# Performance work log

Hardware: AMD Instinct MI355X
Metric: run time of the kernel (lower is better)

## Reference

```python
import jax, jax.numpy as jnp
import numpy as np

N = 100000  # nodes
E = 1600000  # edges (before self-loops)
F_IN, F_HID, F_OUT = 64, 128, 64


def setup_inputs() -> dict:
    key = jax.random.key(0)
    ks = jax.random.split(key, 8)
    x = jax.random.normal(ks[0], (N, F_IN), dtype=jnp.float32)
    edge_index = jax.random.randint(ks[1], (2, E), 0, N, dtype=jnp.int64)
    # Glorot-ish init for weights, zero bias (PyG GCNConv default)
    W1 = jax.random.normal(ks[2], (F_IN, F_HID), dtype=jnp.float32) / np.sqrt(F_IN)
    W2 = jax.random.normal(ks[3], (F_HID, F_HID), dtype=jnp.float32) / np.sqrt(F_HID)
    W3 = jax.random.normal(ks[4], (F_HID, F_OUT), dtype=jnp.float32) / np.sqrt(F_HID)
    b1 = jnp.zeros((F_HID,), dtype=jnp.float32)
    b2 = jnp.zeros((F_HID,), dtype=jnp.float32)
    b3 = jnp.zeros((F_OUT,), dtype=jnp.float32)
    return {"x": x, "edge_index": edge_index, "W1": W1, "b1": b1,
            "W2": W2, "b2": b2, "W3": W3, "b3": b3}


def _gcn_norm(edge_index, num_nodes):
    """Add self-loops and compute symmetric D^-1/2 A D^-1/2 edge norms."""
    loop = jnp.arange(num_nodes, dtype=edge_index.dtype)
    src = jnp.concatenate([edge_index[0], loop])  # [E+N]
    dst = jnp.concatenate([edge_index[1], loop])  # [E+N]
    deg = jax.ops.segment_sum(jnp.ones_like(src, dtype=jnp.float32), dst,
                              num_segments=num_nodes)
    dinv = jnp.where(deg > 0, jax.lax.rsqrt(deg), 0.0)
    norm = dinv[src] * dinv[dst]  # [E+N]
    return src, dst, norm


def _gcn_conv(h, src, dst, norm, W, b, num_nodes):
    hw = h @ W                                   # [N, out] dense transform
    msg = hw[src] * norm[:, None]                # gather + edge scale
    out = jax.ops.segment_sum(msg, dst, num_segments=num_nodes)  # scatter-add
    return out + b


def reference(x, edge_index, W1, b1, W2, b2, W3, b3):
    src, dst, norm = _gcn_norm(edge_index, N)
    h = jax.nn.relu(_gcn_conv(x, src, dst, norm, W1, b1, N))
    h = jax.nn.relu(_gcn_conv(h, src, dst, norm, W2, b2, N))
    return _gcn_conv(h, src, dst, norm, W3, b3, N)
```

## Files before the change

kernel.cpp:

```cpp
#include <hip/hip_runtime.h>
#include <hip/hip_bf16.h>
#include <hip/hip_fp16.h>


typedef _Float16 h8 __attribute__((ext_vector_type(8)));
typedef float f4 __attribute__((ext_vector_type(4)));

constexpr int BSHIFT = 7;
constexpr int BNODES = 1 << BSHIFT;
constexpr int PB     = 256;
constexpr int CAP    = 4096;

__device__ inline void load8h(const _Float16* p, float* f) {
    h8 v = *(const h8*)p;
#pragma unroll
    for (int j = 0; j < 8; j++) f[j] = (float)v[j];
}

__device__ inline void store8h(_Float16* p, const float* f) {
    h8 v;
#pragma unroll
    for (int j = 0; j < 8; j++) v[j] = (_Float16)f[j];
    *(h8*)p = v;
}

__device__ inline void store4h(_Float16* p, float4 v) {
    _Float16 t[4] = {(_Float16)v.x, (_Float16)v.y, (_Float16)v.z, (_Float16)v.w};
    *(uint2*)p = *(uint2*)t;
}

__global__ __launch_bounds__(256) void phist_k(const int* __restrict__ dst,
                                               int* __restrict__ hist,
                                               int E, int nbuck, int chunk) {
    __shared__ int h[1024];
    for (int i = threadIdx.x; i < nbuck; i += 256) h[i] = 0;
    __syncthreads();
    int beg = blockIdx.x * chunk;
    int end = min(E, beg + chunk);
    for (int e = beg + threadIdx.x; e < end; e += 256)
        atomicAdd(&h[dst[e] >> BSHIFT], 1);
    __syncthreads();
    for (int i = threadIdx.x; i < nbuck; i += 256)
        hist[(long)blockIdx.x * nbuck + i] = h[i];
}

__global__ __launch_bounds__(256) void scan_blocks_k(const int* __restrict__ in,
                                                     int* __restrict__ excl,
                                                     int* __restrict__ bsums, int n) {
    __shared__ int s[256];
    int tid = threadIdx.x;
    int i = blockIdx.x * 256 + tid;
    int v = (i < n) ? in[i] : 0;
    s[tid] = v;
    __syncthreads();
    for (int off = 1; off < 256; off <<= 1) {
        int t = (tid >= off) ? s[tid - off] : 0;
        __syncthreads();
        s[tid] += t;
        __syncthreads();
    }
    if (i < n) excl[i] = s[tid] - v;
    if (tid == 255) bsums[blockIdx.x] = s[255];
}

__global__ __launch_bounds__(1024) void mid_k(int* __restrict__ bsums, int nb,
                                              const int* __restrict__ hist,
                                              int* __restrict__ bbase,
                                              int nbuck, int E) {
    __shared__ int s[1024];
    int tid = threadIdx.x;
    int v = 0;
    if (blockIdx.x == 0) {
        v = (tid < nb) ? bsums[tid] : 0;
    } else {
        if (tid < nbuck) {
            int t0 = 0, t1 = 0, t2 = 0, t3 = 0;
            for (int j = 0; j < PB; j += 4) {
                t0 += hist[(long)(j + 0) * nbuck + tid];
                t1 += hist[(long)(j + 1) * nbuck + tid];
                t2 += hist[(long)(j + 2) * nbuck + tid];
                t3 += hist[(long)(j + 3) * nbuck + tid];
            }
            v = (t0 + t1) + (t2 + t3);
        }
    }
    s[tid] = v;
    __syncthreads();
    for (int off = 1; off < 1024; off <<= 1) {
        int t = (tid >= off) ? s[tid - off] : 0;
        __syncthreads();
        s[tid] += t;
        __syncthreads();
    }
    if (blockIdx.x == 0) {
        if (tid < nb) bsums[tid] = s[tid] - v;
    } else {
        if (tid < nbuck) bbase[tid] = s[tid] - v;
        if (tid == 0) bbase[nbuck] = E;
    }
}

__global__ __launch_bounds__(256) void part2_k(const int* __restrict__ src,
                                               const int* __restrict__ dst,
                                               const int* __restrict__ offs,
                                               const int* __restrict__ bsums,
                                               unsigned* __restrict__ ebuf,
                                               int E, int nbuck, int chunk) {
    __shared__ int cur[1024];
    for (int i = threadIdx.x; i < nbuck; i += 256) {
        long flat = (long)blockIdx.x * nbuck + i;
        cur[i] = offs[flat] + bsums[flat >> 8];
    }
    __syncthreads();
    int beg = blockIdx.x * chunk;
    int end = min(E, beg + chunk);
    for (int e = beg + threadIdx.x; e < end; e += 256) {
        int d = dst[e];
        int b = d >> BSHIFT;
        int pos = atomicAdd(&cur[b], 1);
        ebuf[pos] = ((unsigned)(d & (BNODES - 1)) << 25) | (unsigned)src[e];
    }
}

__global__ __launch_bounds__(256) void finalize_k(const unsigned* __restrict__ ebuf,
                                                  const int* __restrict__ hist,
                                                  const int* __restrict__ offs,
                                                  const int* __restrict__ bsums,
                                                  const int* __restrict__ bbase,
                                                  int nbuck,
                                                  int* __restrict__ rowst,
                                                  int* __restrict__ rowend,
                                                  int* __restrict__ midp,
                                                  float* __restrict__ dinv,
                                                  int* __restrict__ col,
                                                  const float* __restrict__ x,
                                                  _Float16* __restrict__ msgX,
                                                  int N, int H) {
    __shared__ unsigned se[CAP];
    __shared__ int cj[PB], sj[PB], sb[PB];
    __shared__ int cnt_s[BNODES], cntA_s[BNODES], scan_s[BNODES];
    __shared__ int cur_s[BNODES], curB_s[BNODES];
    __shared__ float di_s[BNODES];

    int b = blockIdx.x, tid = threadIdx.x;
    int node0 = b << BSHIFT;
    int nn = min(BNODES, N - node0);
    int beg = bbase[b];

    if (tid < PB) {
        long flat = (long)tid * nbuck + b;
        cj[tid] = hist[flat];
        sj[tid] = offs[flat] + bsums[flat >> 8];
    }
    if (tid < BNODES) { cnt_s[tid] = 0; cntA_s[tid] = 0; }
    __syncthreads();

    if (tid < PB) sb[tid] = cj[tid];
    __syncthreads();
    for (int off = 1; off < PB; off <<= 1) {
        int t = 0;
        if (tid < PB && tid >= off) t = sb[tid - off];
        __syncthreads();
        if (tid < PB) sb[tid] += t;
        __syncthreads();
    }
    int m = sb[PB - 1];
    __syncthreads();

    {
        int j = tid;
        int base = sb[j] - cj[j], c = cj[j], s0 = sj[j];
        for (int k = 0; k < c; k++) {
            unsigned e = ebuf[s0 + k];
            int idx = base + k;
            if (idx < CAP) se[idx] = e;
            else {
                atomicAdd(&cnt_s[e >> 25], 1);
                if ((int)(e & 0x1FFFFFFu) < H) atomicAdd(&cntA_s[e >> 25], 1);
            }
        }
    }
    __syncthreads();

    int mcap = m < CAP ? m : CAP;
    for (int i = tid; i < mcap; i += 256) {
        unsigned e = se[i];
        atomicAdd(&cnt_s[e >> 25], 1);
        if ((int)(e & 0x1FFFFFFu) < H) atomicAdd(&cntA_s[e >> 25], 1);
    }
    __syncthreads();

    int v = (tid < BNODES) ? cnt_s[tid] : 0;
    if (tid < BNODES) scan_s[tid] = v;
    __syncthreads();
    for (int off = 1; off < BNODES; off <<= 1) {
        int t = 0;
        if (tid < BNODES && tid >= off) t = scan_s[tid - off];
        __syncthreads();
        if (tid < BNODES) scan_s[tid] += t;
        __syncthreads();
    }
    if (tid < nn) {
        int ex = scan_s[tid] - v;
        int st = beg + ex;
        int ca = cntA_s[tid];
        rowst[node0 + tid] = st;
        rowend[node0 + tid] = st + v;
        midp[node0 + tid] = st + ca;
        float di = rsqrtf((float)v + 1.0f);
        dinv[node0 + tid] = di;
        di_s[tid] = di;
        cur_s[tid] = ex;
        curB_s[tid] = ex + ca;
    }
    __syncthreads();

    for (int i = tid; i < mcap; i += 256) {
        unsigned e = se[i];
        int s = (int)(e & 0x1FFFFFFu), d = e >> 25;
        int p = (s < H) ? atomicAdd(&cur_s[d], 1) : atomicAdd(&curB_s[d], 1);
        col[beg + p] = s;
    }
    if (m > CAP) {
        int j = tid;
        int base = sb[j] - cj[j], c = cj[j], s0 = sj[j];
        for (int k = 0; k < c; k++) {
            int idx = base + k;
            if (idx >= CAP) {
                unsigned e = ebuf[s0 + k];
                int s = (int)(e & 0x1FFFFFFu), d = e >> 25;
                int p = (s < H) ? atomicAdd(&cur_s[d], 1) : atomicAdd(&curB_s[d], 1);
                col[beg + p] = s;
            }
        }
    }

    for (int t = tid; t < nn * 16; t += 256) {
        int nl = t >> 4, q = t & 15;
        int node = node0 + nl;
        float4 vx = *(const float4*)(x + (long)node * 64 + q * 4);
        float di = di_s[nl];
        vx.x *= di; vx.y *= di; vx.z *= di; vx.w *= di;
        store4h(msgX + (long)node * 64 + q * 4, vx);
    }
}

template <int K, int FOUT, bool BIAS, bool RELU, bool DINV_OUT, bool SMOUT>
__global__ __launch_bounds__(256) void fag_k(const _Float16* __restrict__ msg,
                                             const int* __restrict__ rowst,
                                             const int* __restrict__ rowend,
                                             const int* __restrict__ col,
                                             const float* __restrict__ dinv,
                                             const _Float16* __restrict__ Wsw,
                                             const float* __restrict__ bias,
                                             _Float16* __restrict__ C, int n) {
    constexpr int NT = FOUT / 16, NC = K / 32;
    constexpr int LDK = K + 8;
    constexpr int LPN = K / 8;
    constexpr int NPB = 256 / LPN;
    constexpr int CC = 2560;
    __shared__ _Float16 As[64 * LDK];
    __shared__ int cls[CC];

    int tid = threadIdx.x;
    int row0 = blockIdx.x * 64;

    int lastn = min(row0 + 64, n) - 1;
    int beg0 = rowst[row0];
    int win  = rowend[lastn] - beg0;
    int wl = min(win, CC);
    for (int i = tid; i < wl; i += 256) cls[i] = col[beg0 + i];
    __syncthreads();
    const int* cb = (win <= CC) ? (const int*)cls : (col + beg0);

#pragma unroll
    for (int pass = 0; pass < 64 / NPB; pass++) {
        int nl = pass * NPB + tid / LPN;
        int q = tid % LPN;
        int node = row0 + nl;
        float acc[8];
        if (node < n) {
            load8h(msg + (long)node * K + q * 8, acc);
            int beg = rowst[node] - beg0, end = rowend[node] - beg0;
            int e = beg;
            for (; e + 4 <= end; e += 4) {
                int s0 = cb[e], s1 = cb[e + 1], s2 = cb[e + 2], s3 = cb[e + 3];
                h8 v0 = *(const h8*)(msg + (long)s0 * K + q * 8);
                h8 v1 = *(const h8*)(msg + (long)s1 * K + q * 8);
                h8 v2 = *(const h8*)(msg + (long)s2 * K + q * 8);
                h8 v3 = *(const h8*)(msg + (long)s3 * K + q * 8);
#pragma unroll
                for (int j = 0; j < 8; j++)
                    acc[j] += ((float)v0[j] + (float)v1[j]) + ((float)v2[j] + (float)v3[j]);
            }
            for (; e < end; e++) {
                int s = cb[e];
                h8 v = *(const h8*)(msg + (long)s * K + q * 8);
#pragma unroll
                for (int j = 0; j < 8; j++) acc[j] += (float)v[j];
            }
            float di = dinv[node];
#pragma unroll
            for (int j = 0; j < 8; j++) acc[j] *= di;
        } else {
#pragma unroll
            for (int j = 0; j < 8; j++) acc[j] = 0.f;
        }
        h8 o;
#pragma unroll
        for (int j = 0; j < 8; j++) o[j] = (_Float16)acc[j];
        *(h8*)(As + nl * LDK + q * 8) = o;
    }
    __syncthreads();

    int lane = tid & 63, wave = tid >> 6;
    int quad = lane >> 4, cl = lane & 15;
    int r0 = wave * 16;

    h8 a[NC];
#pragma unroll
    for (int c = 0; c < NC; c++)
        a[c] = *(const h8*)(As + (r0 + cl) * LDK + quad * 8 + c * 32);

    f4 acc2[NT];
#pragma unroll
    for (int t = 0; t < NT; t++) acc2[t] = (f4){0.f, 0.f, 0.f, 0.f};

    const h8* wv = (const h8*)Wsw;
#pragma unroll
    for (int c = 0; c < NC; c++) {
#pragma unroll
        for (int t = 0; t < NT; t++)
            acc2[t] = __builtin_amdgcn_mfma_f32_16x16x32_f16(
                a[c], wv[(c * NT + t) * 64 + lane], acc2[t], 0, 0, 0);
    }

#pragma unroll
    for (int t = 0; t < NT; t++) {
        int c0 = t * 16 + cl;
        float bb = BIAS ? bias[c0] : 0.f;
#pragma unroll
        for (int r = 0; r < 4; r++) {
            int row = row0 + r0 + quad * 4 + r;
            if (row >= n) continue;
            float v = acc2[t][r] + bb;
            if (RELU) v = fmaxf(v, 0.f);
            if (DINV_OUT) v *= dinv[row];
            if (SMOUT)
                C[((long)(t >> 1) * n + row) * 32 + (t & 1) * 16 + cl] = (_Float16)v;
            else
                C[(long)row * FOUT + c0] = (_Float16)v;
        }
    }
}

__global__ __launch_bounds__(256) void agg_h2_k(const _Float16* __restrict__ msg,
                                                const int* __restrict__ rowst,
                                                const int* __restrict__ midp,
                                                const int* __restrict__ rowend,
                                                const int* __restrict__ col,
                                                _Float16* __restrict__ part, int n) {
    constexpr int CC = 1536;
    __shared__ int cls[CC];
    int idx7  = blockIdx.x & 7;
    int slice = idx7 & 3, half = idx7 >> 2;
    int blk   = blockIdx.x >> 3;
    int tid   = threadIdx.x;
    int node0b = blk * 32;

    int lastn = min(node0b + 32, n) - 1;
    int beg0 = rowst[node0b];
    int win  = rowend[lastn] - beg0;
    int wl = min(win, CC);
    for (int i = tid; i < wl; i += 256) cls[i] = col[beg0 + i];
    __syncthreads();
    const int* cb = (win <= CC) ? (const int*)cls : (col + beg0);

    int node  = node0b + (tid >> 3);
    int eslot = (tid >> 2) & 1;
    int q     = tid & 3;
    if (node >= n) return;
    const _Float16* mp = msg + (long)slice * n * 32 + q * 8;

    float acc[8];
#pragma unroll
    for (int j = 0; j < 8; j++) acc[j] = 0.f;

    int beg = (half ? midp[node] : rowst[node]) - beg0;
    int end = (half ? rowend[node] : midp[node]) - beg0;
    int e = beg + eslot;
    for (; e + 6 < end; e += 8) {
        int s0 = cb[e], s1 = cb[e + 2], s2 = cb[e + 4], s3 = cb[e + 6];
        h8 v0 = *(const h8*)(mp + (long)s0 * 32);
        h8 v1 = *(const h8*)(mp + (long)s1 * 32);
        h8 v2 = *(const h8*)(mp + (long)s2 * 32);
        h8 v3 = *(const h8*)(mp + (long)s3 * 32);
#pragma unroll
        for (int j = 0; j < 8; j++)
            acc[j] += (((float)v0[j] + (float)v1[j]) + ((float)v2[j] + (float)v3[j]));
    }
    for (; e < end; e += 2) {
        int s = cb[e];
        h8 v = *(const h8*)(mp + (long)s * 32);
#pragma unroll
        for (int j = 0; j < 8; j++) acc[j] += (float)v[j];
    }

#pragma unroll
    for (int j = 0; j < 8; j++) acc[j] += __shfl_xor(acc[j], 4);

    if (eslot == 0) {
        store8h(part + (((long)half * 4 + slice) * n + node) * 32 + q * 8, acc);
    }
}

template <int F, bool BIAS, bool F16OUT>
__global__ __launch_bounds__(256) void agg_f16_k(const _Float16* __restrict__ msg,
                                                 const int* __restrict__ rowst,
                                                 const int* __restrict__ rowend,
                                                 const int* __restrict__ col,
                                                 const float* __restrict__ dinv,
                                                 const float* __restrict__ b,
                                                 void* __restrict__ out, int n) {
    constexpr int LPN = F / 8;
    constexpr int NPB = 256 / LPN;
    constexpr int CC = NPB * 48;
    __shared__ int cls[CC];
    int tid = threadIdx.x;
    int node0b = blockIdx.x * NPB;

    int lastn = min(node0b + NPB, n) - 1;
    int beg0 = rowst[node0b];
    int win  = rowend[lastn] - beg0;
    int wl = min(win, CC);
    for (int i = tid; i < wl; i += 256) cls[i] = col[beg0 + i];
    __syncthreads();
    const int* cb = (win <= CC) ? (const int*)cls : (col + beg0);

    int node = node0b + tid / LPN;
    int q = tid % LPN;
    if (node >= n) return;

    float acc[8];
    load8h(msg + (long)node * F + q * 8, acc);

    int beg = rowst[node] - beg0, end = rowend[node] - beg0;
    int e = beg;
    for (; e + 8 <= end; e += 8) {
        h8 v[8];
#pragma unroll
        for (int u = 0; u < 8; u++)
            v[u] = *(const h8*)(msg + (long)cb[e + u] * F + q * 8);
#pragma unroll
        for (int j = 0; j < 8; j++)
            acc[j] += (((float)v[0][j] + (float)v[1][j]) + ((float)v[2][j] + (float)v[3][j])) +
                      (((float)v[4][j] + (float)v[5][j]) + ((float)v[6][j] + (float)v[7][j]));
    }
    for (; e + 4 <= end; e += 4) {
        h8 v0 = *(const h8*)(msg + (long)cb[e] * F + q * 8);
        h8 v1 = *(const h8*)(msg + (long)cb[e + 1] * F + q * 8);
        h8 v2 = *(const h8*)(msg + (long)cb[e + 2] * F + q * 8);
        h8 v3 = *(const h8*)(msg + (long)cb[e + 3] * F + q * 8);
#pragma unroll
        for (int j = 0; j < 8; j++)
            acc[j] += ((float)v0[j] + (float)v1[j]) + ((float)v2[j] + (float)v3[j]);
    }
    for (; e < end; e++) {
        h8 v = *(const h8*)(msg + (long)cb[e] * F + q * 8);
#pragma unroll
        for (int j = 0; j < 8; j++) acc[j] += (float)v[j];
    }

    float di = dinv[node];
    float o[8];
#pragma unroll
    for (int j = 0; j < 8; j++) o[j] = di * acc[j];
    if (BIAS) {
#pragma unroll
        for (int j = 0; j < 8; j++) o[j] += b[q * 8 + j];
    }
    if (F16OUT) {
        store8h((_Float16*)out + (long)node * F + q * 8, o);
    } else {
        float* dst = (float*)out + (long)node * F + q * 8;
        *(float4*)dst = make_float4(o[0], o[1], o[2], o[3]);
        *(float4*)(dst + 4) = make_float4(o[4], o[5], o[6], o[7]);
    }
}

template <int K, int FOUT>
__device__ inline void wfrag(const float* __restrict__ W,
                             _Float16* __restrict__ Wsw, int t) {
    constexpr int NT = FOUT / 16;
    int lane = t & 63;
    int tile = (t >> 6) % NT;
    int chunk = (t >> 6) / NT;
    int kbase = chunk * 32 + (lane >> 4) * 8;
    int nc = tile * 16 + (lane & 15);
    h8 v;
#pragma unroll
    for (int j = 0; j < 8; j++) v[j] = (_Float16)W[(kbase + j) * FOUT + nc];
    ((h8*)Wsw)[t] = v;
}

__global__ __launch_bounds__(256) void wprep3_k(const float* __restrict__ W1,
                                                const float* __restrict__ W2,
                                                const float* __restrict__ W3,
                                                _Float16* __restrict__ w1s,
                                                _Float16* __restrict__ w2s,
                                                _Float16* __restrict__ w3s) {
    int t = blockIdx.x * 256 + threadIdx.x;
    if (t < 1024) wfrag<64, 128>(W1, w1s, t);
    else if (t < 3072) wfrag<128, 128>(W2, w2s, t - 1024);
    else if (t < 4096) wfrag<128, 64>(W3, w3s, t - 3072);
}

__global__ __launch_bounds__(256) void dgemm_k(const _Float16* __restrict__ part,
                                               const _Float16* __restrict__ selfm,
                                               const _Float16* __restrict__ w2s,
                                               const _Float16* __restrict__ w3s,
                                               const float* __restrict__ b2,
                                               const float* __restrict__ dinv,
                                               _Float16* __restrict__ C, int n) {
    constexpr int LDK = 136;
    __shared__ _Float16 Hs[64 * LDK];

    int tid = threadIdx.x, lane = tid & 63, wave = tid >> 6;
    int quad = lane >> 4, cl = lane & 15;
    int row0 = blockIdx.x * 64, r0 = wave * 16;
    int arow = row0 + r0 + cl;

    const _Float16* pA = part;
    const _Float16* pB = part + (long)4 * n * 32;
    float di = dinv[arow];

    h8 a[4];
#pragma unroll
    for (int c = 0; c < 4; c++) {
        long off = ((long)c * n + arow) * 32 + quad * 8;
        h8 va = *(const h8*)(pA + off);
        h8 vb = *(const h8*)(pB + off);
        h8 vs = *(const h8*)(selfm + off);
        h8 o;
#pragma unroll
        for (int j = 0; j < 8; j++) {
            float f = (((float)va[j] + (float)vb[j]) + (float)vs[j]) * di;
            o[j] = (_Float16)f;
        }
        a[c] = o;
    }

    f4 acc1[8];
#pragma unroll
    for (int t = 0; t < 8; t++) acc1[t] = (f4){0.f, 0.f, 0.f, 0.f};
    const h8* wv2 = (const h8*)w2s;
#pragma unroll
    for (int c = 0; c < 4; c++) {
#pragma unroll
        for (int t = 0; t < 8; t++)
            acc1[t] = __builtin_amdgcn_mfma_f32_16x16x32_f16(
                a[c], wv2[(c * 8 + t) * 64 + lane], acc1[t], 0, 0, 0);
    }

#pragma unroll
    for (int t = 0; t < 8; t++) {
        int c0 = t * 16 + cl;
        float bb = b2[c0];
#pragma unroll
        for (int r = 0; r < 4; r++) {
            float v = fmaxf(acc1[t][r] + bb, 0.f);
            Hs[(r0 + quad * 4 + r) * LDK + c0] = (_Float16)v;
        }
    }
    __builtin_amdgcn_s_waitcnt(0);

    h8 a2[4];
#pragma unroll
    for (int c = 0; c < 4; c++)
        a2[c] = *(const h8*)(Hs + (r0 + cl) * LDK + quad * 8 + c * 32);

    f4 acc2[4];
#pragma unroll
    for (int t = 0; t < 4; t++) acc2[t] = (f4){0.f, 0.f, 0.f, 0.f};
    const h8* wv3 = (const h8*)w3s;
#pragma unroll
    for (int c = 0; c < 4; c++) {
#pragma unroll
        for (int t = 0; t < 4; t++)
            acc2[t] = __builtin_amdgcn_mfma_f32_16x16x32_f16(
                a2[c], wv3[(c * 4 + t) * 64 + lane], acc2[t], 0, 0, 0);
    }

#pragma unroll
    for (int t = 0; t < 4; t++) {
        int c0 = t * 16 + cl;
#pragma unroll
        for (int r = 0; r < 4; r++) {
            int row = row0 + r0 + quad * 4 + r;
            if (row >= n) continue;
            float v = acc2[t][r] * dinv[row];
            C[(long)row * 64 + c0] = (_Float16)v;
        }
    }
}

extern "C" void kernel_launch(void* const* d_in, const int* in_sizes, int n_in,
                              void* d_out, int out_size, void* d_ws, size_t ws_size,
                              hipStream_t stream) {
    const float* x  = (const float*)d_in[0];
    const int*   ei = (const int*)d_in[1];
    const float* W1 = (const float*)d_in[2];
    const float* b1 = (const float*)d_in[3];
    const float* W2 = (const float*)d_in[4];
    const float* b2 = (const float*)d_in[5];
    const float* W3 = (const float*)d_in[6];
    const float* b3 = (const float*)d_in[7];
    float* out = (float*)d_out;

    const int N = in_sizes[0] / 64;
    const int E = in_sizes[1] / 2;
    const int* src = ei;
    const int* dst = ei + E;
    const int nbuck = (N + BNODES - 1) >> BSHIFT;
    const int chunk = (E + PB - 1) / PB;
    const int n2 = PB * nbuck;
    const int nb2 = (n2 + 255) / 256;

    int*   hist   = (int*)d_ws;
    int*   offs   = hist + n2;
    int*   bsums  = offs + n2;
    int*   bbase  = bsums + 1024;
    int*   rowst  = bbase + nbuck + 1;
    int*   rowend = rowst + N;
    float* dinv   = (float*)(rowend + N);
    int*   col    = (int*)(dinv + N);
    _Float16* w1s = (_Float16*)(col + E);
    _Float16* w2s = w1s + 64 * 128;
    _Float16* w3s = w2s + 128 * 128;
    float* P      = (float*)(w3s + 128 * 64);
    float* Q      = P + (long)N * 128;

    _Float16* msgX  = (_Float16*)P;
    _Float16* part  = (_Float16*)P;
    unsigned* ebuf  = (unsigned*)Q;
    _Float16* msg1  = (_Float16*)Q;
    _Float16* msg3  = (_Float16*)(Q + (long)N * 64);
    int*      midp  = (int*)(Q + (long)N * 96);

    const int gb = (N + 63) / 64;

    wprep3_k<<<16, 256, 0, stream>>>(W1, W2, W3, w1s, w2s, w3s);

    phist_k<<<PB, 256, 0, stream>>>(dst, hist, E, nbuck, chunk);
    scan_blocks_k<<<nb2, 256, 0, stream>>>(hist, offs, bsums, n2);
    mid_k<<<2, 1024, 0, stream>>>(bsums, nb2, hist, bbase, nbuck, E);
    part2_k<<<PB, 256, 0, stream>>>(src, dst, offs, bsums, ebuf, E, nbuck, chunk);
    finalize_k<<<nbuck, 256, 0, stream>>>(ebuf, hist, offs, bsums, bbase, nbuck,
                                          rowst, rowend, midp, dinv, col, x,
                                          msgX, N, N / 2);

    fag_k<64, 128, true, true, true, true><<<gb, 256, 0, stream>>>(
        msgX, rowst, rowend, col, dinv, w1s, b1, msg1, N);

    const int nb32 = (N + 31) / 32;
    agg_h2_k<<<8 * nb32, 256, 0, stream>>>(
        msg1, rowst, midp, rowend, col, part, N);

    dgemm_k<<<gb, 256, 0, stream>>>(part, msg1, w2s, w3s, b2, dinv, msg3, N);

    agg_f16_k<64, true, false><<<(N + 31) / 32, 256, 0, stream>>>(
        msg3, rowst, rowend, col, dinv, b3, (void*)out, N);
}
```

Measured before the change: 364.0 us.

## Split layer-1 aggregation into sliced partial-sum kernel plus separate GEMM kernel

Layer 1's fused aggregate-then-GEMM kernel is replaced by two kernels, mirroring the layer-2 path. The input messages are stored in a feature-sliced layout (two 32-wide slices) so gathers touch 64-byte rows. Each node's edge list is split into halves at the midpoint, with each half handled by a separate block and two threads per node interleaving edges. A new GEMM kernel then sums the partials and the self term, scales by dinv, and applies W1, bias, ReLU and output scaling. This aims for more parallelism and better gather locality in the edge loop, at the cost of an extra launch and a partial-sum buffer written and read back through memory.

```diff
diff --git a/kernel.cpp b/kernel.cpp
--- a/kernel.cpp
+++ b/kernel.cpp
@@ -241,115 +241,123 @@
         float4 vx = *(const float4*)(x + (long)node * 64 + q * 4);
         float di = di_s[nl];
         vx.x *= di; vx.y *= di; vx.z *= di; vx.w *= di;
-        store4h(msgX + (long)node * 64 + q * 4, vx);
-    }
-}
-
-template <int K, int FOUT, bool BIAS, bool RELU, bool DINV_OUT, bool SMOUT>
-__global__ __launch_bounds__(256) void fag_k(const _Float16* __restrict__ msg,
-                                             const int* __restrict__ rowst,
-                                             const int* __restrict__ rowend,
-                                             const int* __restrict__ col,
-                                             const float* __restrict__ dinv,
-                                             const _Float16* __restrict__ Wsw,
-                                             const float* __restrict__ bias,
-                                             _Float16* __restrict__ C, int n) {
-    constexpr int NT = FOUT / 16, NC = K / 32;
-    constexpr int LDK = K + 8;
-    constexpr int LPN = K / 8;
-    constexpr int NPB = 256 / LPN;
-    constexpr int CC = 2560;
-    __shared__ _Float16 As[64 * LDK];
+        int sl = q >> 3, ps = (q & 7) * 4;
+        store4h(msgX + ((long)sl * N + node) * 32 + ps, vx);
+    }
+}
+
+__global__ __launch_bounds__(256) void agg_h1_k(const _Float16* __restrict__ msg,
+                                                const int* __restrict__ rowst,
+                                                const int* __restrict__ midp,
+                                                const int* __restrict__ rowend,
+                                                const int* __restrict__ col,
+                                                _Float16* __restrict__ part, int n) {
+    constexpr int CC = 1536;
     __shared__ int cls[CC];
-
-    int tid = threadIdx.x;
-    int row0 = blockIdx.x * 64;
-
-    int lastn = min(row0 + 64, n) - 1;
-    int beg0 = rowst[row0];
+    int idx7  = blockIdx.x & 7;
+    int slice = idx7 & 1, half = (idx7 >> 1) & 1, nh = idx7 >> 2;
+    int blk   = ((blockIdx.x >> 3) << 1) + nh;
+    int tid   = threadIdx.x;
+    int node0b = blk * 32;
+    if (node0b >= n) return;
+
+    int lastn = min(node0b + 32, n) - 1;
+    int beg0 = rowst[node0b];
     int win  = rowend[lastn] - beg0;
     int wl = min(win, CC);
     for (int i = tid; i < wl; i += 256) cls[i] = col[beg0 + i];
     __syncthreads();
     const int* cb = (win <= CC) ? (const int*)cls : (col + beg0);
 
-#pragma unroll
-    for (int pass = 0; pass < 64 / NPB; pass++) {
-        int nl = pass * NPB + tid / LPN;
-        int q = tid % LPN;
-        int node = row0 + nl;
-        float acc[8];
-        if (node < n) {
-            load8h(msg + (long)node * K + q * 8, acc);
-            int beg = rowst[node] - beg0, end = rowend[node] - beg0;
-            int e = beg;
-            for (; e + 4 <= end; e += 4) {
-                int s0 = cb[e], s1 = cb[e + 1], s2 = cb[e + 2], s3 = cb[e + 3];
-                h8 v0 = *(const h8*)(msg + (long)s0 * K + q * 8);
-                h8 v1 = *(const h8*)(msg + (long)s1 * K + q * 8);
-                h8 v2 = *(const h8*)(msg + (long)s2 * K + q * 8);
-                h8 v3 = *(const h8*)(msg + (long)s3 * K + q * 8);
-#pragma unroll
-                for (int j = 0; j < 8; j++)
-                    acc[j] += ((float)v0[j] + (float)v1[j]) + ((float)v2[j] + (float)v3[j]);
-            }
-            for (; e < end; e++) {
-                int s = cb[e];
-                h8 v = *(const h8*)(msg + (long)s * K + q * 8);
-#pragma unroll
-                for (int j = 0; j < 8; j++) acc[j] += (float)v[j];
-            }
-            float di = dinv[node];
-#pragma unroll
-            for (int j = 0; j < 8; j++) acc[j] *= di;
-        } else {
-#pragma unroll
-            for (int j = 0; j < 8; j++) acc[j] = 0.f;
-        }
+    int node  = node0b + (tid >> 3);
+    int eslot = (tid >> 2) & 1;
+    int q     = tid & 3;
+    if (node >= n) return;
+    const _Float16* mp = msg + (long)slice * n * 32 + q * 8;
+
+    float acc[8];
+#pragma unroll
+    for (int j = 0; j < 8; j++) acc[j] = 0.f;
+
+    int beg = (half ? midp[node] : rowst[node]) - beg0;
+    int end = (half ? rowend[node] : midp[node]) - beg0;
+    int e = beg + eslot;
+    for (; e + 6 < end; e += 8) {
+        int s0 = cb[e], s1 = cb[e + 2], s2 = cb[e + 4], s3 = cb[e + 6];
+        h8 v0 = *(const h8*)(mp + (long)s0 * 32);
+        h8 v1 = *(const h8*)(mp + (long)s1 * 32);
+        h8 v2 = *(const h8*)(mp + (long)s2 * 32);
+        h8 v3 = *(const h8*)(mp + (long)s3 * 32);
+#pragma unroll
+        for (int j = 0; j < 8; j++)
+            acc[j] += (((float)v0[j] + (float)v1[j]) + ((float)v2[j] + (float)v3[j]));
+    }
+    for (; e < end; e += 2) {
+        int s = cb[e];
+        h8 v = *(const h8*)(mp + (long)s * 32);
+#pragma unroll
+        for (int j = 0; j < 8; j++) acc[j] += (float)v[j];
+    }
+
+#pragma unroll
+    for (int j = 0; j < 8; j++) acc[j] += __shfl_xor(acc[j], 4);
+
+    if (eslot == 0) {
+        store8h(part + (((long)half * 2 + slice) * n + node) * 32 + q * 8, acc);
+    }
+}
+
+__global__ __launch_bounds__(256) void fagc_k(const _Float16* __restrict__ part,
+                                              const _Float16* __restrict__ selfm,
+                                              const float* __restrict__ dinv,
+                                              const _Float16* __restrict__ w1s,
+                                              const float* __restrict__ b1,
+                                              _Float16* __restrict__ C, int n) {
+    int tid = threadIdx.x, lane = tid & 63, wave = tid >> 6;
+    int quad = lane >> 4, cl = lane & 15;
+    int row0 = blockIdx.x * 64, r0 = wave * 16;
+    int arow = row0 + r0 + cl;
+
+    float di = dinv[arow];
+
+    h8 a[2];
+#pragma unroll
+    for (int c = 0; c < 2; c++) {
+        long off = ((long)c * n + arow) * 32 + quad * 8;
+        h8 v0 = *(const h8*)(part + off);
+        h8 v1 = *(const h8*)(part + (long)2 * n * 32 + off);
+        h8 vs = *(const h8*)(selfm + off);
         h8 o;
 #pragma unroll
-        for (int j = 0; j < 8; j++) o[j] = (_Float16)acc[j];
-        *(h8*)(As + nl * LDK + q * 8) = o;
-    }
-    __syncthreads();
-
-    int lane = tid & 63, wave = tid >> 6;
-    int quad = lane >> 4, cl = lane & 15;
-    int r0 = wave * 16;
-
-    h8 a[NC];
-#pragma unroll
-    for (int c = 0; c < NC; c++)
-        a[c] = *(const h8*)(As + (r0 + cl) * LDK + quad * 8 + c * 32);
-
-    f4 acc2[NT];
-#pragma unroll
-    for (int t = 0; t < NT; t++) acc2[t] = (f4){0.f, 0.f, 0.f, 0.f};
-
-    const h8* wv = (const h8*)Wsw;
-#pragma unroll
-    for (int c = 0; c < NC; c++) {
-#pragma unroll
-        for (int t = 0; t < NT; t++)
-            acc2[t] = __builtin_amdgcn_mfma_f32_16x16x32_f16(
-                a[c], wv[(c * NT + t) * 64 + lane], acc2[t], 0, 0, 0);
-    }
-
-#pragma unroll
-    for (int t = 0; t < NT; t++) {
+        for (int j = 0; j < 8; j++) {
+            float f = (((float)v0[j] + (float)v1[j]) + (float)vs[j]) * di;
+            o[j] = (_Float16)f;
+        }
+        a[c] = o;
+    }
+
+    f4 acc[8];
+#pragma unroll
+    for (int t = 0; t < 8; t++) acc[t] = (f4){0.f, 0.f, 0.f, 0.f};
+    const h8* wv = (const h8*)w1s;
+#pragma unroll
+    for (int c = 0; c < 2; c++) {
+#pragma unroll
+        for (int t = 0; t < 8; t++)
+            acc[t] = __builtin_amdgcn_mfma_f32_16x16x32_f16(
+                a[c], wv[(c * 8 + t) * 64 + lane], acc[t], 0, 0, 0);
+    }
+
+#pragma unroll
+    for (int t = 0; t < 8; t++) {
         int c0 = t * 16 + cl;
-        float bb = BIAS ? bias[c0] : 0.f;
+        float bb = b1[c0];
 #pragma unroll
         for (int r = 0; r < 4; r++) {
             int row = row0 + r0 + quad * 4 + r;
             if (row >= n) continue;
-            float v = acc2[t][r] + bb;
-            if (RELU) v = fmaxf(v, 0.f);
-            if (DINV_OUT) v *= dinv[row];
-            if (SMOUT)
-                C[((long)(t >> 1) * n + row) * 32 + (t & 1) * 16 + cl] = (_Float16)v;
-            else
-                C[(long)row * FOUT + c0] = (_Float16)v;
+            float v = fmaxf(acc[t][r] + bb, 0.f) * dinv[row];
+            C[((long)(t >> 1) * n + row) * 32 + (t & 1) * 16 + cl] = (_Float16)v;
         }
     }
 }
@@ -640,8 +648,9 @@
     float* P      = (float*)(w3s + 128 * 64);
     float* Q      = P + (long)N * 128;
 
-    _Float16* msgX  = (_Float16*)P;
-    _Float16* part  = (_Float16*)P;
+    _Float16* msgXs = (_Float16*)P;
+    _Float16* part1 = msgXs + (long)N * 64;
+    _Float16* part2 = (_Float16*)P;
     unsigned* ebuf  = (unsigned*)Q;
     _Float16* msg1  = (_Float16*)Q;
     _Float16* msg3  = (_Float16*)(Q + (long)N * 64);
@@ -657,16 +666,19 @@
     part2_k<<<PB, 256, 0, stream>>>(src, dst, offs, bsums, ebuf, E, nbuck, chunk);
     finalize_k<<<nbuck, 256, 0, stream>>>(ebuf, hist, offs, bsums, bbase, nbuck,
                                           rowst, rowend, midp, dinv, col, x,
-                                          msgX, N, N / 2);
-
-    fag_k<64, 128, true, true, true, true><<<gb, 256, 0, stream>>>(
-        msgX, rowst, rowend, col, dinv, w1s, b1, msg1, N);
+                                          msgXs, N, N / 2);
+
+    const int nbh = ((N + 31) / 32 + 1) / 2;
+    agg_h1_k<<<8 * nbh, 256, 0, stream>>>(
+        msgXs, rowst, midp, rowend, col, part1, N);
+
+    fagc_k<<<gb, 256, 0, stream>>>(part1, msgXs, dinv, w1s, b1, msg1, N);
 
     const int nb32 = (N + 31) / 32;
     agg_h2_k<<<8 * nb32, 256, 0, stream>>>(
-        msg1, rowst, midp, rowend, col, part, N);
-
-    dgemm_k<<<gb, 256, 0, stream>>>(part, msg1, w2s, w3s, b2, dinv, msg3, N);
+        msg1, rowst, midp, rowend, col, part2, N);
+
+    dgemm_k<<<gb, 256, 0, stream>>>(part2, msg1, w2s, w3s, b2, dinv, msg3, N);
 
     agg_f16_k<64, true, false><<<(N + 31) / 32, 256, 0, stream>>>(
         msg3, rowst, rowend, col, dinv, b3, (void*)out, N);
```

New measurement: 359.5 us. About the same (-1.2%).
